# Kernel optimization log

Hardware: AMD Instinct MI355X
Metric: run time of the kernel (lower is better)

Reference implementation:

```python
import jax, jax.numpy as jnp
import numpy as np

B, T, D, H = 64, 512, 256, 1024


def setup_inputs() -> dict:
    key = jax.random.key(0)
    ks = jax.random.split(key, 4)
    def xavier(k, shape):
        fan_in, fan_out = shape[1], shape[0]
        lim = np.sqrt(6.0 / (fan_in + fan_out)).astype(np.float32)
        return jax.random.uniform(k, shape, jnp.float32, -lim, lim)
    inputs = jax.random.normal(ks[0], (B, T, D), dtype=jnp.float32)
    Wx = xavier(ks[1], (4 * H, D))      # x2h weight
    bx = jnp.zeros((4 * H,), jnp.float32)
    Wh = xavier(ks[2], (4 * H, H))      # h2h weight
    bh = jnp.zeros((4 * H,), jnp.float32)
    Wout = xavier(ks[3], (D, H))        # output head
    bout = jnp.zeros((D,), jnp.float32)
    return {"inputs": inputs, "Wx": Wx, "bx": bx, "Wh": Wh, "bh": bh,
            "Wout": Wout, "bout": bout}


def _lstm_seq(inputs, Wx, bx, Wh, bh):
    # Precompute input-to-hidden gates for all timesteps: (T, B, 4H)
    xg = jnp.einsum('btd,gd->tbg', inputs, Wx) + bx
    h0 = jnp.zeros((inputs.shape[0], H), inputs.dtype)
    c0 = jnp.zeros_like(h0)

    def step(carry, xg_t):
        h, c = carry
        gates = xg_t + h @ Wh.T + bh            # (B, 4H)
        i, f, g, o = jnp.split(jax.nn.sigmoid(gates), 4, axis=-1)
        # NOTE: source applies sigmoid to the cell gate too (not tanh)
        c = c * f + i * g
        h = o * jnp.tanh(c)
        return (h, c), h

    _, hs = jax.lax.scan(step, (h0, c0), xg)    # hs: (T, B, H)
    return jnp.transpose(hs, (1, 0, 2))         # (B, T, H)


def reference(inputs, Wx, bx, Wh, bh, Wout, bout):
    hs = _lstm_seq(inputs, Wx, bx, Wh, bh)      # (B, T, H)
    # Faithful to source: output head uses raw hiddens; returned hidden is tanh'd
    out = jnp.einsum('bth,dh->btd', hs, Wout) + bout
    hidden = jnp.tanh(hs)
    return out, hidden
```

## Files before the change

### kernel.cpp

```cpp
#include <hip/hip_runtime.h>
#include <math.h>

#define BB 64
#define TT 512
#define DD 256
#define HH 1024
#define GG 4096

typedef __bf16 bf16x8 __attribute__((ext_vector_type(8)));
typedef float floatx4 __attribute__((ext_vector_type(4)));
typedef unsigned int u32x4 __attribute__((ext_vector_type(4)));
typedef unsigned long long u64;

__global__ void cvt_bf16_kernel(const float* __restrict__ src,
                                __bf16* __restrict__ dst, int n) {
    int i = (blockIdx.x * blockDim.x + threadIdx.x) * 8;
    if (i >= n) return;
    float4 a = *(const float4*)(src + i);
    float4 b = *(const float4*)(src + i + 4);
    bf16x8 v;
    v[0] = (__bf16)a.x; v[1] = (__bf16)a.y; v[2] = (__bf16)a.z; v[3] = (__bf16)a.w;
    v[4] = (__bf16)b.x; v[5] = (__bf16)b.y; v[6] = (__bf16)b.z; v[7] = (__bf16)b.w;
    *(bf16x8*)(dst + i) = v;
}

__global__ void init_misc_kernel(const float* __restrict__ bx,
                                 const float* __restrict__ bh,
                                 float* __restrict__ bc,
                                 unsigned* __restrict__ flags) {
    int i = blockIdx.x * blockDim.x + threadIdx.x;
    if (i < GG) bc[i] = bx[i] + bh[i];
    if (i < 1024) flags[i] = 0u;
}

__global__ __launch_bounds__(1024, 1) void lstm_seq_kernel(
    const float* __restrict__ x,
    const __bf16* __restrict__ Wxb,
    const __bf16* __restrict__ Whb,
    const float* __restrict__ bc,
    float* __restrict__ hs,
    __bf16* __restrict__ hping,
    unsigned* __restrict__ flags) {
    __shared__ __bf16 W_s[16][1288];
    __shared__ float gate_s[4][64][18];

    const int tid = threadIdx.x;
    const int bid = blockIdx.x;
    const int j0 = bid * 4;

    for (int ch = tid; ch < 2560; ch += 1024) {
        int r = ch / 160;
        int pos = ch - r * 160;
        int k = pos * 8;
        int gate = r >> 2;
        int jr = r & 3;
        int gr = gate * HH + j0 + jr;
        const __bf16* src = (k < DD) ? (Wxb + (size_t)gr * DD + k)
                                     : (Whb + (size_t)gr * HH + (k - DD));
        *(uint4*)(&W_s[r][k]) = *(const uint4*)src;
    }

    const int wave = tid >> 6;
    const int lane = tid & 63;
    const int kg = wave >> 2;
    const int bw = wave & 3;
    const int ln = lane & 15;
    const int q = lane >> 4;
    const int brow = bw * 16 + ln;
    const int xk0 = kg * 64;
    const int hk0 = kg * 256;

    const int b2 = tid >> 2;
    const int jj = tid & 3;
    const int j = j0 + jj;
    const float bci = bc[j];
    const float bcf = bc[HH + j];
    const float bcg = bc[2 * HH + j];
    const float bco = bc[3 * HH + j];
    float creg = 0.0f;

    __syncthreads();

    for (int t = 0; t < TT; ++t) {
        floatx4 acc = {0.f, 0.f, 0.f, 0.f};

        {
            const float* xrow = x + ((size_t)brow * TT + t) * DD;
#pragma unroll
            for (int i = 0; i < 2; ++i) {
                int ka = xk0 + 32 * i + q * 8;
                float4 f0 = *(const float4*)(xrow + ka);
                float4 f1 = *(const float4*)(xrow + ka + 4);
                bf16x8 av;
                av[0] = (__bf16)f0.x; av[1] = (__bf16)f0.y;
                av[2] = (__bf16)f0.z; av[3] = (__bf16)f0.w;
                av[4] = (__bf16)f1.x; av[5] = (__bf16)f1.y;
                av[6] = (__bf16)f1.z; av[7] = (__bf16)f1.w;
                bf16x8 bv = *(const bf16x8*)(&W_s[ln][ka]);
                acc = __builtin_amdgcn_mfma_f32_16x16x32_bf16(av, bv, acc, 0, 0, 0);
            }
        }

        if (t > 0) {
            if (tid >= 960) {
                const unsigned tgt = (unsigned)t;
                const u32x4* fp = (const u32x4*)flags + (tid - 960);
                for (;;) {
                    u32x4 v;
                    asm volatile(
                        "global_load_dwordx4 %0, %1, off sc1\n\t"
                        "s_waitcnt vmcnt(0)"
                        : "=v"(v) : "v"(fp) : "memory");
                    bool ok = (v[0] >= tgt) && (v[1] >= tgt) &&
                              (v[2] >= tgt) && (v[3] >= tgt);
                    if (__all((int)ok)) break;
                    __builtin_amdgcn_s_sleep(1);
                }
                __threadfence();
            }
            __syncthreads();

            const __bf16* hrow = hping + (size_t)((t - 1) & 1) * (BB * HH) +
                                 (size_t)brow * HH + hk0 + q * 8;
            bf16x8 hv[8];
#pragma unroll
            for (int i = 0; i < 8; ++i)
                hv[i] = *(const bf16x8*)(hrow + 32 * i);
            __builtin_amdgcn_sched_barrier(0);
#pragma unroll
            for (int i = 0; i < 8; ++i) {
                bf16x8 bv = *(const bf16x8*)(&W_s[ln][DD + hk0 + 32 * i + q * 8]);
                acc = __builtin_amdgcn_mfma_f32_16x16x32_bf16(hv[i], bv, acc, 0, 0, 0);
            }
        }

#pragma unroll
        for (int r = 0; r < 4; ++r)
            gate_s[kg][bw * 16 + q * 4 + r][ln] = acc[r];
        __syncthreads();

        floatx4 f4 = {0.f, 0.f, 0.f, 0.f};
        bool st = false;
        if (tid < 256) {
            float iv = gate_s[0][b2][jj] + gate_s[1][b2][jj] +
                       gate_s[2][b2][jj] + gate_s[3][b2][jj] + bci;
            float fv = gate_s[0][b2][4 + jj] + gate_s[1][b2][4 + jj] +
                       gate_s[2][b2][4 + jj] + gate_s[3][b2][4 + jj] + bcf;
            float gv = gate_s[0][b2][8 + jj] + gate_s[1][b2][8 + jj] +
                       gate_s[2][b2][8 + jj] + gate_s[3][b2][8 + jj] + bcg;
            float ov = gate_s[0][b2][12 + jj] + gate_s[1][b2][12 + jj] +
                       gate_s[2][b2][12 + jj] + gate_s[3][b2][12 + jj] + bco;
            iv = 1.f / (1.f + expf(-iv));
            fv = 1.f / (1.f + expf(-fv));
            gv = 1.f / (1.f + expf(-gv));
            ov = 1.f / (1.f + expf(-ov));
            creg = creg * fv + iv * gv;
            float hh = ov * tanhf(creg);

            int base = lane & ~3;
            float h0 = __shfl(hh, base);
            float h1 = __shfl(hh, base + 1);
            float h2 = __shfl(hh, base + 2);
            float h3 = __shfl(hh, base + 3);
            if (jj == 0) {
                st = true;
                f4[0] = h0; f4[1] = h1; f4[2] = h2; f4[3] = h3;
                if (t < TT - 1) {
                    unsigned short s0 = __builtin_bit_cast(unsigned short, (__bf16)h0);
                    unsigned short s1 = __builtin_bit_cast(unsigned short, (__bf16)h1);
                    unsigned short s2 = __builtin_bit_cast(unsigned short, (__bf16)h2);
                    unsigned short s3 = __builtin_bit_cast(unsigned short, (__bf16)h3);
                    u64 pk = (u64)s0 | ((u64)s1 << 16) | ((u64)s2 << 32) |
                             ((u64)s3 << 48);
                    __hip_atomic_store(
                        (u64*)(hping + (size_t)(t & 1) * (BB * HH) +
                               (size_t)b2 * HH + j0),
                        pk, __ATOMIC_RELAXED, __HIP_MEMORY_SCOPE_AGENT);
                }
            }
        }

        float* hsp = hs + ((size_t)b2 * TT + t) * HH + j0;
        if (t == TT - 1) {
            if (st) *(floatx4*)hsp = f4;
            break;
        }

        asm volatile("s_waitcnt vmcnt(0)" ::: "memory");
        __syncthreads();
        if (tid == 0)
            __hip_atomic_store(flags + bid, (unsigned)(t + 1),
                               __ATOMIC_RELAXED, __HIP_MEMORY_SCOPE_AGENT);
        if (st)
            asm volatile("global_store_dwordx4 %0, %1, off sc1"
                         :: "v"(hsp), "v"(f4) : "memory");
    }
}

__global__ __launch_bounds__(256) void out_gemm_kernel(
    const float* __restrict__ hs,
    const __bf16* __restrict__ Wob,
    const float* __restrict__ bout,
    float* __restrict__ out) {
    __shared__ __bf16 Wout_s[16][1032];
    const int tid = threadIdx.x;
    const int d0 = blockIdx.x * 16;
    const int row0 = blockIdx.y * 64;

    for (int ch = tid; ch < 2048; ch += 256) {
        int r = ch >> 7;
        int k = (ch & 127) * 8;
        *(uint4*)(&Wout_s[r][k]) = *(const uint4*)(Wob + (size_t)(d0 + r) * HH + k);
    }
    __syncthreads();

    const int wave = tid >> 6;
    const int lane = tid & 63;
    const int ln = lane & 15;
    const int q = lane >> 4;
    const int row = row0 + wave * 16 + ln;

    const float* arow = hs + (size_t)row * HH;
    floatx4 acc = {0.f, 0.f, 0.f, 0.f};
#pragma unroll 8
    for (int k0 = 0; k0 < HH; k0 += 32) {
        int ka = k0 + q * 8;
        float4 f0 = *(const float4*)(arow + ka);
        float4 f1 = *(const float4*)(arow + ka + 4);
        bf16x8 av;
        av[0] = (__bf16)f0.x; av[1] = (__bf16)f0.y;
        av[2] = (__bf16)f0.z; av[3] = (__bf16)f0.w;
        av[4] = (__bf16)f1.x; av[5] = (__bf16)f1.y;
        av[6] = (__bf16)f1.z; av[7] = (__bf16)f1.w;
        bf16x8 bv = *(const bf16x8*)(&Wout_s[ln][ka]);
        acc = __builtin_amdgcn_mfma_f32_16x16x32_bf16(av, bv, acc, 0, 0, 0);
    }
    float bo = bout[d0 + ln];
    const int orow0 = row0 + wave * 16 + q * 4;
#pragma unroll
    for (int r = 0; r < 4; ++r)
        out[(size_t)(orow0 + r) * DD + d0 + ln] = acc[r] + bo;
}

__global__ void tanh_inplace_kernel(float* __restrict__ p, size_t n) {
    size_t i = ((size_t)blockIdx.x * blockDim.x + threadIdx.x) * 4;
    size_t stride = (size_t)gridDim.x * blockDim.x * 4;
    for (; i < n; i += stride) {
        float4 v = *(float4*)(p + i);
        v.x = tanhf(v.x); v.y = tanhf(v.y); v.z = tanhf(v.z); v.w = tanhf(v.w);
        *(float4*)(p + i) = v;
    }
}

extern "C" void kernel_launch(void* const* d_in, const int* in_sizes, int n_in,
                              void* d_out, int out_size, void* d_ws, size_t ws_size,
                              hipStream_t stream) {
    const float* x    = (const float*)d_in[0];
    const float* Wx   = (const float*)d_in[1];
    const float* bx   = (const float*)d_in[2];
    const float* Wh   = (const float*)d_in[3];
    const float* bh   = (const float*)d_in[4];
    const float* Wout = (const float*)d_in[5];
    const float* bout = (const float*)d_in[6];

    float* out = (float*)d_out;
    float* hidden = out + (size_t)BB * TT * DD;

    char* ws = (char*)d_ws;
    __bf16* Wxb   = (__bf16*)(ws);
    __bf16* Whb   = (__bf16*)(ws + 2097152);
    __bf16* Wob   = (__bf16*)(ws + 10485760);
    float*  bc    = (float*)(ws + 11010048);
    unsigned* flg = (unsigned*)(ws + 11026432);
    __bf16* hping = (__bf16*)(ws + 11288576);

    cvt_bf16_kernel<<<(GG * DD / 8 + 255) / 256, 256, 0, stream>>>(Wx, Wxb, GG * DD);
    cvt_bf16_kernel<<<(GG * HH / 8 + 255) / 256, 256, 0, stream>>>(Wh, Whb, GG * HH);
    cvt_bf16_kernel<<<(DD * HH / 8 + 255) / 256, 256, 0, stream>>>(Wout, Wob, DD * HH);
    init_misc_kernel<<<(GG + 255) / 256, 256, 0, stream>>>(bx, bh, bc, flg);

    {
        const float* xp = x;
        const __bf16* wxp = Wxb;
        const __bf16* whp = Whb;
        const float* bcp = bc;
        float* hsp = hidden;
        __bf16* hpp = hping;
        unsigned* flp = flg;
        void* kargs[] = {(void*)&xp, (void*)&wxp, (void*)&whp, (void*)&bcp,
                         (void*)&hsp, (void*)&hpp, (void*)&flp};
        (void)hipLaunchCooperativeKernel(reinterpret_cast<void*>(lstm_seq_kernel),
                                         dim3(256), dim3(1024), kargs, 0, stream);
    }

    out_gemm_kernel<<<dim3(DD / 16, (BB * TT) / 64), 256, 0, stream>>>(
        hidden, Wob, bout, out);
    tanh_inplace_kernel<<<2048, 256, 0, stream>>>(hidden, (size_t)BB * TT * HH);
}
```

Baseline: 6.253 ms.

## Use hierarchical epoch barrier, swizzle weight LDS layout, move hs store before flag wait

Replaces the all-to-all flag polling, where every block reads all 256 flags, with a two-level scheme. Block 0 polls all flags and then publishes an epoch word, while the other blocks poll only that single word. This cuts global polling traffic but adds a relay hop of latency on every step. It also changes the weight layout in shared memory to a chunk-interleaved one to avoid bank conflicts on MFMA operand reads. Finally, the hs output store now issues before the vmcnt wait, so it is included in the wait before the flag release.

Measured after the change: 6.399 ms. 2.3% more time.

```diff
diff --git a/kernel.cpp b/kernel.cpp
--- a/kernel.cpp
+++ b/kernel.cpp
@@ -41,23 +41,26 @@
     float* __restrict__ hs,
     __bf16* __restrict__ hping,
     unsigned* __restrict__ flags) {
-    __shared__ __bf16 W_s[16][1288];
+    __shared__ __bf16 W_s[40 * 512];
     __shared__ float gate_s[4][64][18];
 
     const int tid = threadIdx.x;
     const int bid = blockIdx.x;
     const int j0 = bid * 4;
+    unsigned* const epoch = flags + 512;
 
     for (int ch = tid; ch < 2560; ch += 1024) {
         int r = ch / 160;
-        int pos = ch - r * 160;
-        int k = pos * 8;
+        int c8 = ch - r * 160;
+        int k = c8 * 8;
         int gate = r >> 2;
         int jr = r & 3;
         int gr = gate * HH + j0 + jr;
         const __bf16* src = (k < DD) ? (Wxb + (size_t)gr * DD + k)
                                      : (Whb + (size_t)gr * HH + (k - DD));
-        *(uint4*)(&W_s[r][k]) = *(const uint4*)src;
+        int c = c8 >> 2;
+        int q = c8 & 3;
+        *(uint4*)(&W_s[(c * 64 + q * 16 + r) * 8]) = *(const uint4*)src;
     }
 
     const int wave = tid >> 6;
@@ -96,7 +99,7 @@
                 av[2] = (__bf16)f0.z; av[3] = (__bf16)f0.w;
                 av[4] = (__bf16)f1.x; av[5] = (__bf16)f1.y;
                 av[6] = (__bf16)f1.z; av[7] = (__bf16)f1.w;
-                bf16x8 bv = *(const bf16x8*)(&W_s[ln][ka]);
+                bf16x8 bv = *(const bf16x8*)(&W_s[((kg * 2 + i) * 64 + q * 16 + ln) * 8]);
                 acc = __builtin_amdgcn_mfma_f32_16x16x32_bf16(av, bv, acc, 0, 0, 0);
             }
         }
@@ -104,17 +107,32 @@
         if (t > 0) {
             if (tid >= 960) {
                 const unsigned tgt = (unsigned)t;
-                const u32x4* fp = (const u32x4*)flags + (tid - 960);
-                for (;;) {
-                    u32x4 v;
-                    asm volatile(
-                        "global_load_dwordx4 %0, %1, off sc1\n\t"
-                        "s_waitcnt vmcnt(0)"
-                        : "=v"(v) : "v"(fp) : "memory");
-                    bool ok = (v[0] >= tgt) && (v[1] >= tgt) &&
-                              (v[2] >= tgt) && (v[3] >= tgt);
-                    if (__all((int)ok)) break;
-                    __builtin_amdgcn_s_sleep(1);
+                if (bid == 0) {
+                    const u32x4* fp = (const u32x4*)flags + lane;
+                    for (;;) {
+                        u32x4 v;
+                        asm volatile(
+                            "global_load_dwordx4 %0, %1, off sc1\n\t"
+                            "s_waitcnt vmcnt(0)"
+                            : "=v"(v) : "v"(fp) : "memory");
+                        bool ok = (v[0] >= tgt) && (v[1] >= tgt) &&
+                                  (v[2] >= tgt) && (v[3] >= tgt);
+                        if (__all((int)ok)) break;
+                        __builtin_amdgcn_s_sleep(1);
+                    }
+                    if (lane == 0)
+                        __hip_atomic_store(epoch, tgt, __ATOMIC_RELAXED,
+                                           __HIP_MEMORY_SCOPE_AGENT);
+                } else {
+                    for (;;) {
+                        unsigned v;
+                        asm volatile(
+                            "global_load_dword %0, %1, off sc1\n\t"
+                            "s_waitcnt vmcnt(0)"
+                            : "=v"(v) : "v"(epoch) : "memory");
+                        if (v >= tgt) break;
+                        __builtin_amdgcn_s_sleep(1);
+                    }
                 }
                 __threadfence();
             }
@@ -129,7 +147,7 @@
             __builtin_amdgcn_sched_barrier(0);
 #pragma unroll
             for (int i = 0; i < 8; ++i) {
-                bf16x8 bv = *(const bf16x8*)(&W_s[ln][DD + hk0 + 32 * i + q * 8]);
+                bf16x8 bv = *(const bf16x8*)(&W_s[((8 + kg * 8 + i) * 64 + q * 16 + ln) * 8]);
                 acc = __builtin_amdgcn_mfma_f32_16x16x32_bf16(hv[i], bv, acc, 0, 0, 0);
             }
         }
@@ -185,15 +203,15 @@
             if (st) *(floatx4*)hsp = f4;
             break;
         }
+        if (st)
+            asm volatile("global_store_dwordx4 %0, %1, off sc1"
+                         :: "v"(hsp), "v"(f4) : "memory");
 
         asm volatile("s_waitcnt vmcnt(0)" ::: "memory");
         __syncthreads();
         if (tid == 0)
             __hip_atomic_store(flags + bid, (unsigned)(t + 1),
                                __ATOMIC_RELAXED, __HIP_MEMORY_SCOPE_AGENT);
-        if (st)
-            asm volatile("global_store_dwordx4 %0, %1, off sc1"
-                         :: "v"(hsp), "v"(f4) : "memory");
     }
 }
 
```
